# Optimization experiments

Hardware: AMD Instinct MI355X
Metric: run time of the kernel (lower is better)

Reference implementation:

```python
import jax, jax.numpy as jnp
import numpy as np

B, L, D = 4, 2048, 2048
H, KVH = 16, 4
HD = D // H            # 128
G = H // KVH           # GQA group size
K_SEL = L // 4         # top_k_ratio = 0.25 -> 512
MAX_SEQ = 8192
THETA = 10000.0
SCALE = HD ** -0.5
NEG = -1e9


def _rope_tables(dim, max_len, theta):
    inv = 1.0 / theta ** (jnp.arange(0, dim, 2, dtype=jnp.float32) / dim)  # (dim/2,)
    ang = jnp.arange(max_len, dtype=jnp.float32)[:, None] * inv[None, :]   # (max_len, dim/2)
    return jnp.cos(ang), jnp.sin(ang)


def _apply_rope_pos(x, cos, sin, pos):
    # x: (B, h, K, HD), pos: (B, K) int positions
    c = cos[pos][:, None]  # (B,1,K,HD/2)
    s = sin[pos][:, None]
    x1, x2 = jnp.split(x, 2, axis=-1)
    return jnp.concatenate([x1 * c - x2 * s, x1 * s + x2 * c], axis=-1)


def setup_inputs() -> dict:
    key = jax.random.key(0)
    ks = jax.random.split(key, 8)
    std = 0.02
    x   = jax.random.normal(ks[0], (B, L, D), dtype=jnp.float32)
    Wq  = jax.random.normal(ks[1], (D, D), dtype=jnp.float32) * std
    Wkv = jax.random.normal(ks[2], (D, 2 * KVH * HD), dtype=jnp.float32) * std
    Wo  = jax.random.normal(ks[3], (D, D), dtype=jnp.float32) * std
    W1  = jax.random.normal(ks[4], (D, D // 4), dtype=jnp.float32) * std
    b1  = jnp.zeros((D // 4,), dtype=jnp.float32)
    W2  = jax.random.normal(ks[5], (D // 4, 1), dtype=jnp.float32) * std
    b2  = jnp.zeros((1,), dtype=jnp.float32)
    return {"x": x, "Wq": Wq, "Wkv": Wkv, "Wo": Wo,
            "W1": W1, "b1": b1, "W2": W2, "b2": b2}


def reference(x, Wq, Wkv, Wo, W1, b1, W2, b2):
    Bx, Lx, Dx = x.shape
    # 1. learned per-token importance scores
    imp = (jax.nn.gelu(x @ W1 + b1, approximate=False) @ W2 + b2)[..., 0]  # (B,L)
    # 2. top-k token selection, sorted to keep original order
    _, idx = jax.lax.top_k(imp, K_SEL)
    idx = jnp.sort(idx, axis=-1)                                           # (B,K)
    x_sel = jnp.take_along_axis(x, idx[..., None], axis=1)                 # (B,K,D)
    # 3. fused KV projection on the selected subset (GQA)
    kv = x_sel @ Wkv
    k, v = jnp.split(kv, 2, axis=-1)
    k = k.reshape(Bx, K_SEL, KVH, HD).transpose(0, 2, 1, 3)                # (B,KVH,K,HD)
    v = v.reshape(Bx, K_SEL, KVH, HD).transpose(0, 2, 1, 3)
    # 4. RoPE with original positions for K, contiguous positions for Q
    cos, sin = _rope_tables(HD, MAX_SEQ, THETA)
    k = _apply_rope_pos(k, cos, sin, idx)
    q = (x @ Wq).reshape(Bx, Lx, H, HD).transpose(0, 2, 1, 3)              # (B,H,L,HD)
    qpos = jnp.broadcast_to(jnp.arange(Lx)[None, :], (Bx, Lx))
    q = _apply_rope_pos(q, cos, sin, qpos)
    # 5. GQA head expansion + attention over gathered keys
    k = jnp.repeat(k, G, axis=1)                                           # (B,H,K,HD)
    v = jnp.repeat(v, G, axis=1)
    scores = jnp.einsum('bhld,bhkd->bhlk', q, k) * SCALE                   # (B,H,L,K)
    # causal mask on original key positions
    causal = idx[:, None, None, :] > jnp.arange(Lx)[None, None, :, None]
    scores = jnp.where(causal, NEG, scores)
    attn = jax.nn.softmax(scores, axis=-1)
    # 6. importance soft gating (gradient path into the scorer)
    gate = jax.nn.sigmoid(jnp.take_along_axis(imp, idx, axis=1))           # (B,K)
    attn = attn * gate[:, None, None, :]
    out = jnp.einsum('bhlk,bhkd->bhld', attn, v)                           # (B,H,L,HD)
    out = out.transpose(0, 2, 1, 3).reshape(Bx, Lx, Dx)
    return out @ Wo
```

## Files before the change

kernel.cpp:

```cpp
#include <hip/hip_runtime.h>
#include <math.h>

typedef unsigned short u16;
typedef __attribute__((ext_vector_type(8))) short short8;
typedef __attribute__((ext_vector_type(4))) float f32x4;

__device__ __forceinline__ float bf2f(u16 u) {
  return __uint_as_float(((unsigned)u) << 16);
}
__device__ __forceinline__ u16 f2bf(float f) {
  unsigned u = __float_as_uint(f);
  return (u16)((u + 0x7fffu + ((u >> 16) & 1u)) >> 16);
}

__device__ __forceinline__ void gload_lds16(const u16* g, u16* l) {
  __builtin_amdgcn_global_load_lds((const __attribute__((address_space(1))) unsigned int*)g,
                                   (__attribute__((address_space(3))) unsigned int*)l, 16, 0, 0);
}

__device__ __forceinline__ void stage_tile(const u16* __restrict__ gbase, int ldg,
                                           u16* lds, int w, int lane) {
  #pragma unroll
  for (int i = 0; i < 4; ++i) {
    int c = w * 4 + i;
    const u16* g = gbase + (size_t)(c * 8 + (lane >> 3)) * ldg + (lane & 7) * 8;
    gload_lds16(g, lds + c * 512);
  }
}

__global__ __launch_bounds__(256) void cvt_x_kernel(const float* __restrict__ x,
                                                    u16* __restrict__ xb,
                                                    u16* __restrict__ xlo) {
  size_t base = ((size_t)blockIdx.x * 256 + threadIdx.x) * 8;
  short8 hi, lo;
  #pragma unroll
  for (int i = 0; i < 8; ++i) {
    float v = x[base + i];
    u16 h = f2bf(v);
    hi[i] = (short)h;
    lo[i] = (short)f2bf(v - bf2f(h));
  }
  *(short8*)&xb[base] = hi;
  *(short8*)&xlo[base] = lo;
}

template <bool HILO>
__global__ __launch_bounds__(256) void transpose_cvt(const float* __restrict__ in,
                                                     u16* __restrict__ outH,
                                                     u16* __restrict__ outL,
                                                     int R, int C) {
  __shared__ u16 tH[64][72];
  __shared__ u16 tL[64][72];
  int rb = blockIdx.y * 64, cb = blockIdx.x * 64;
  int t = threadIdx.x;
  #pragma unroll
  for (int i = 0; i < 16; ++i) {
    int r = i * 4 + (t >> 6), c = t & 63;
    float v = in[(size_t)(rb + r) * C + cb + c];
    u16 h = f2bf(v);
    tH[r][c] = h;
    if (HILO) tL[r][c] = f2bf(v - bf2f(h));
  }
  __syncthreads();
  #pragma unroll
  for (int i = 0; i < 16; ++i) {
    int r = i * 4 + (t >> 6), c = t & 63;
    outH[(size_t)(cb + r) * R + rb + c] = tH[c][r];
    if (HILO) outL[(size_t)(cb + r) * R + rb + c] = tL[c][r];
  }
}

__global__ void ropetab_kernel(float* __restrict__ cosT, float* __restrict__ sinT) {
  int pos = blockIdx.x, i = threadIdx.x;
  float e = (float)(2 * i) * (1.0f / 128.0f);
  float inv = powf(10000.0f, -e);
  float ang = (float)pos * inv;
  cosT[pos * 64 + i] = cosf(ang);
  sinT[pos * 64 + i] = sinf(ang);
}

template <bool BF16OUT>
__global__ __launch_bounds__(512, 2) void gemm256(const u16* __restrict__ A,
                                                  const u16* __restrict__ BT,
                                                  float* __restrict__ Cf,
                                                  u16* __restrict__ Cb,
                                                  int M, int N, int K) {
  __shared__ __align__(1024) u16 smem[65536];
  const int bm = blockIdx.x * 256, bn = blockIdx.y * 256;
  const int t = threadIdx.x, lane = t & 63, w = t >> 6;
  const int ll = lane & 15, lh = lane >> 4;
  const int wr = w >> 2, wc = w & 3;
  const int NT = K >> 6;

  const int tt0 = t, tt1 = t + 512;
  const int r0 = tt0 >> 2, r1 = tt1 >> 2;
  const int c0 = (((tt0 & 3) ^ ((tt0 >> 3) & 3)) << 3);
  const int c1 = (((tt1 & 3) ^ ((tt1 >> 3) & 3)) << 3);
  const size_t aoff0 = (size_t)(bm + r0) * K + c0;
  const size_t aoff1 = (size_t)(bm + r1) * K + c1;
  const size_t boff0 = (size_t)(bn + r0) * K + c0;
  const size_t boff1 = (size_t)(bn + r1) * K + c1;

  const int swz = ((lh ^ ((ll >> 1) & 3)) << 3);
  const int arow = (wr * 128 + ll) * 32 + swz;
  const int brow = (wc * 64 + ll) * 32 + swz;

  f32x4 acc[8][4];
  #pragma unroll
  for (int mi = 0; mi < 8; ++mi)
    #pragma unroll
    for (int ni = 0; ni < 4; ++ni) acc[mi][ni] = f32x4{0.f, 0.f, 0.f, 0.f};

  short8 aq[8], bq[2];

#define G_STAGE(base, o0, o1, lds) \
  gload_lds16((base) + (o0), (lds) + w * 512); \
  gload_lds16((base) + (o1), (lds) + 4096 + w * 512)
#define RD_A(Sa, ks) \
  _Pragma("unroll") for (int mi = 0; mi < 8; ++mi) aq[mi] = *(const short8*)&(Sa)[(ks)*8192 + arow + mi * 512]
#define RD_B(Sb, ks, nh) \
  _Pragma("unroll") for (int n2 = 0; n2 < 2; ++n2) bq[n2] = *(const short8*)&(Sb)[(ks)*8192 + brow + ((nh)*2 + n2) * 512]
#define DO_MFMA(nh) \
  __builtin_amdgcn_s_setprio(1); \
  _Pragma("unroll") for (int mi = 0; mi < 8; ++mi) \
    _Pragma("unroll") for (int n2 = 0; n2 < 2; ++n2) \
      acc[mi][(nh)*2 + n2] = __builtin_amdgcn_mfma_f32_16x16x32_bf16(aq[mi], bq[n2], acc[mi][(nh)*2 + n2], 0, 0, 0); \
  __builtin_amdgcn_s_setprio(0)
#define VMW(n) asm volatile("s_waitcnt vmcnt(" #n ")" ::: "memory")

  G_STAGE(A, aoff0, aoff1, smem);
  G_STAGE(BT, boff0, boff1, smem + 16384);
  G_STAGE(A, aoff0 + 32, aoff1 + 32, smem + 8192);
  G_STAGE(BT, boff0 + 32, boff1 + 32, smem + 16384 + 8192);

  for (int kt = 0; kt < NT - 1; ++kt) {
    const int cur = kt & 1;
    u16* Sa = smem + cur * 32768;
    u16* Sb = Sa + 16384;
    u16* Pa = smem + (cur ^ 1) * 32768;
    u16* Pb = Pa + 16384;
    const size_t kg = (size_t)(kt + 1) * 64;
    VMW(4);
    __builtin_amdgcn_s_barrier();
    G_STAGE(A, aoff0 + kg, aoff1 + kg, Pa);
    RD_A(Sa, 0);
    RD_B(Sb, 0, 0);
    DO_MFMA(0);
    __builtin_amdgcn_s_barrier();
    G_STAGE(BT, boff0 + kg, boff1 + kg, Pb);
    RD_B(Sb, 0, 1);
    DO_MFMA(1);
    VMW(4);
    __builtin_amdgcn_s_barrier();
    G_STAGE(A, aoff0 + kg + 32, aoff1 + kg + 32, Pa + 8192);
    RD_A(Sa, 1);
    RD_B(Sb, 1, 0);
    DO_MFMA(0);
    __builtin_amdgcn_s_barrier();
    G_STAGE(BT, boff0 + kg + 32, boff1 + kg + 32, Pb + 8192);
    RD_B(Sb, 1, 1);
    DO_MFMA(1);
  }
  {
    const int cur = (NT - 1) & 1;
    u16* Sa = smem + cur * 32768;
    u16* Sb = Sa + 16384;
    VMW(4);
    __builtin_amdgcn_s_barrier();
    RD_A(Sa, 0); RD_B(Sb, 0, 0); DO_MFMA(0);
    __builtin_amdgcn_s_barrier();
    RD_B(Sb, 0, 1); DO_MFMA(1);
    VMW(0);
    __builtin_amdgcn_s_barrier();
    RD_A(Sa, 1); RD_B(Sb, 1, 0); DO_MFMA(0);
    __builtin_amdgcn_s_barrier();
    RD_B(Sb, 1, 1); DO_MFMA(1);
  }

  #pragma unroll
  for (int mi = 0; mi < 8; ++mi)
    #pragma unroll
    for (int ni = 0; ni < 4; ++ni)
      #pragma unroll
      for (int r = 0; r < 4; ++r) {
        int row = bm + wr * 128 + mi * 16 + lh * 4 + r;
        int col = bn + wc * 64 + ni * 16 + ll;
        float v = acc[mi][ni][r];
        if (BF16OUT) Cb[(size_t)row * N + col] = f2bf(v);
        else Cf[(size_t)row * N + col] = v;
      }
#undef G_STAGE
#undef RD_A
#undef RD_B
#undef DO_MFMA
#undef VMW
}

__global__ __launch_bounds__(256) void gemm_bt_gather(const u16* __restrict__ A,
                                                      const u16* __restrict__ BT,
                                                      const int* __restrict__ rowidx,
                                                      float* __restrict__ Cpart,
                                                      int M, int N, int K) {
  constexpr int BK = 64;
  __shared__ u16 As[128][BK + 8];
  __shared__ u16 Bs[128][BK + 8];
  const int bm = blockIdx.x * 128, bn = blockIdx.y * 128;
  const int kz = blockIdx.z;
  const int t = threadIdx.x, lane = t & 63, w = t >> 6;
  const int lh = lane >> 4, ll = lane & 15;
  const int wm = (w >> 1) * 64, wn = (w & 1) * 64;
  f32x4 acc[4][4];
  #pragma unroll
  for (int mt = 0; mt < 4; ++mt)
    #pragma unroll
    for (int nt = 0; nt < 4; ++nt) acc[mt][nt] = f32x4{0.f, 0.f, 0.f, 0.f};

  const int k0 = kz * (K / 2), k1 = k0 + K / 2;
  for (int kb = k0; kb < k1; kb += BK) {
    __syncthreads();
    #pragma unroll
    for (int i = 0; i < 4; ++i) {
      int e = t + i * 256;
      int row = e >> 3, c8 = e & 7;
      int arow = rowidx[bm + row];
      *(short8*)&As[row][c8 * 8] = *(const short8*)&A[(size_t)arow * K + kb + c8 * 8];
      *(short8*)&Bs[row][c8 * 8] = *(const short8*)&BT[(size_t)(bn + row) * K + kb + c8 * 8];
    }
    __syncthreads();
    #pragma unroll
    for (int ks = 0; ks < 2; ++ks) {
      short8 a[4], b[4];
      #pragma unroll
      for (int mt = 0; mt < 4; ++mt) a[mt] = *(const short8*)&As[wm + mt * 16 + ll][ks * 32 + lh * 8];
      #pragma unroll
      for (int nt = 0; nt < 4; ++nt) b[nt] = *(const short8*)&Bs[wn + nt * 16 + ll][ks * 32 + lh * 8];
      #pragma unroll
      for (int mt = 0; mt < 4; ++mt)
        #pragma unroll
        for (int nt = 0; nt < 4; ++nt)
          acc[mt][nt] = __builtin_amdgcn_mfma_f32_16x16x32_bf16(a[mt], b[nt], acc[mt][nt], 0, 0, 0);
    }
  }
  float* C = Cpart + (size_t)kz * M * N;
  #pragma unroll
  for (int mt = 0; mt < 4; ++mt)
    #pragma unroll
    for (int nt = 0; nt < 4; ++nt)
      #pragma unroll
      for (int r = 0; r < 4; ++r) {
        int row = bm + wm + mt * 16 + lh * 4 + r;
        int col = bn + wn + nt * 16 + ll;
        C[(size_t)row * N + col] = acc[mt][nt][r];
      }
}

__global__ __launch_bounds__(256) void gemm_scorer(const u16* __restrict__ Ahi,
                                                   const u16* __restrict__ Alo,
                                                   const u16* __restrict__ Bhi,
                                                   const u16* __restrict__ Blo,
                                                   float* __restrict__ Cpart,
                                                   int M, int N, int K) {
  __shared__ __align__(1024) u16 smem[4 * 128 * 64];
  u16* AsH = smem;
  u16* AsL = smem + 128 * 64;
  u16* BsH = smem + 2 * 128 * 64;
  u16* BsL = smem + 3 * 128 * 64;
  const int bm = blockIdx.x * 128, bn = blockIdx.y * 128;
  const int kz = blockIdx.z;
  const int t = threadIdx.x, lane = t & 63, w = t >> 6;
  const int lh = lane >> 4, ll = lane & 15;
  const int wm = (w >> 1) * 64, wn = (w & 1) * 64;
  f32x4 acc[4][4];
  #pragma unroll
  for (int mt = 0; mt < 4; ++mt)
    #pragma unroll
    for (int nt = 0; nt < 4; ++nt) acc[mt][nt] = f32x4{0.f, 0.f, 0.f, 0.f};

  const int k0 = kz * (K / 2), k1 = k0 + K / 2;
  for (int kb = k0; kb < k1; kb += 64) {
    __syncthreads();
    stage_tile(Ahi + (size_t)bm * K + kb, K, AsH, w, lane);
    stage_tile(Alo + (size_t)bm * K + kb, K, AsL, w, lane);
    stage_tile(Bhi + (size_t)bn * K + kb, K, BsH, w, lane);
    stage_tile(Blo + (size_t)bn * K + kb, K, BsL, w, lane);
    __syncthreads();
    #pragma unroll
    for (int ks = 0; ks < 2; ++ks) {
      short8 ah[4], al[4], bh[4], bl[4];
      #pragma unroll
      for (int mt = 0; mt < 4; ++mt) {
        int o = (wm + mt * 16 + ll) * 64 + ks * 32 + lh * 8;
        ah[mt] = *(const short8*)&AsH[o];
        al[mt] = *(const short8*)&AsL[o];
      }
      #pragma unroll
      for (int nt = 0; nt < 4; ++nt) {
        int o = (wn + nt * 16 + ll) * 64 + ks * 32 + lh * 8;
        bh[nt] = *(const short8*)&BsH[o];
        bl[nt] = *(const short8*)&BsL[o];
      }
      #pragma unroll
      for (int mt = 0; mt < 4; ++mt)
        #pragma unroll
        for (int nt = 0; nt < 4; ++nt) {
          acc[mt][nt] = __builtin_amdgcn_mfma_f32_16x16x32_bf16(ah[mt], bh[nt], acc[mt][nt], 0, 0, 0);
          acc[mt][nt] = __builtin_amdgcn_mfma_f32_16x16x32_bf16(ah[mt], bl[nt], acc[mt][nt], 0, 0, 0);
          acc[mt][nt] = __builtin_amdgcn_mfma_f32_16x16x32_bf16(al[mt], bh[nt], acc[mt][nt], 0, 0, 0);
        }
    }
  }
  float* C = Cpart + (size_t)kz * M * N;
  #pragma unroll
  for (int mt = 0; mt < 4; ++mt)
    #pragma unroll
    for (int nt = 0; nt < 4; ++nt)
      #pragma unroll
      for (int r = 0; r < 4; ++r) {
        int row = bm + wm + mt * 16 + lh * 4 + r;
        int col = bn + wn + nt * 16 + ll;
        C[(size_t)row * N + col] = acc[mt][nt][r];
      }
}

__global__ __launch_bounds__(256) void scorer_finish(const float* __restrict__ hg,
                                                     const float* __restrict__ b1,
                                                     const float* __restrict__ W2,
                                                     const float* __restrict__ b2,
                                                     float* __restrict__ imp) {
  int tok = blockIdx.x * 4 + (threadIdx.x >> 6);
  int lane = threadIdx.x & 63;
  const float* h0 = hg + (size_t)tok * 512;
  const float* h1 = hg + (size_t)8192 * 512 + (size_t)tok * 512;
  float s = 0.f;
  #pragma unroll
  for (int i = 0; i < 8; ++i) {
    int c = lane + i * 64;
    float v = h0[c] + h1[c] + b1[c];
    v = 0.5f * v * (1.0f + erff(v * 0.70710678118654752f));
    s += v * W2[c];
  }
  #pragma unroll
  for (int off = 32; off; off >>= 1) s += __shfl_xor(s, off, 64);
  if (lane == 0) imp[tok] = s + b2[0];
}

__global__ __launch_bounds__(1024) void topk_kernel(const float* __restrict__ imp,
                                                    int* __restrict__ idx_sel,
                                                    int* __restrict__ sel_rows,
                                                    float* __restrict__ gatev) {
  __shared__ float v[2048];
  __shared__ int ix[2048];
  __shared__ int ids[512];
  int b = blockIdx.x, t = threadIdx.x;
  for (int i = t; i < 2048; i += 1024) { v[i] = imp[b * 2048 + i]; ix[i] = i; }
  __syncthreads();
  for (int k = 2; k <= 2048; k <<= 1)
    for (int j = k >> 1; j > 0; j >>= 1) {
      int i = ((t & ~(j - 1)) << 1) | (t & (j - 1));
      int l2 = i | j;
      bool dir = ((i & k) == 0);
      float vi = v[i], vl = v[l2];
      int xi = ix[i], xl = ix[l2];
      bool g = (vi < vl) || (vi == vl && xi > xl);
      if (g == dir) { v[i] = vl; v[l2] = vi; ix[i] = xl; ix[l2] = xi; }
      __syncthreads();
    }
  if (t < 512) ids[t] = ix[t];
  __syncthreads();
  for (int k = 2; k <= 512; k <<= 1)
    for (int j = k >> 1; j > 0; j >>= 1) {
      if (t < 256) {
        int i = ((t & ~(j - 1)) << 1) | (t & (j - 1));
        int l2 = i | j;
        bool dir = ((i & k) == 0);
        int ai = ids[i], al = ids[l2];
        if ((ai > al) == dir) { ids[i] = al; ids[l2] = ai; }
      }
      __syncthreads();
    }
  if (t < 512) {
    int id = ids[t];
    idx_sel[b * 512 + t] = id;
    sel_rows[b * 512 + t] = b * 2048 + id;
    float g = imp[b * 2048 + id];
    gatev[b * 512 + t] = 1.0f / (1.0f + __expf(-g));
  }
}

__global__ __launch_bounds__(256) void rope_k2(const float* __restrict__ part,
                                               const int* __restrict__ idx_sel,
                                               const float* __restrict__ cosT,
                                               const float* __restrict__ sinT,
                                               u16* __restrict__ Kb) {
  int gid = blockIdx.x * 256 + threadIdx.x;
  int i = gid & 63;
  int s = (gid >> 6) & 511;
  int kvh = (gid >> 15) & 3;
  int b = gid >> 17;
  size_t src = (size_t)(b * 512 + s) * 1024 + kvh * 128 + i;
  float k1 = part[src] + part[src + 2097152];
  float k2 = part[src + 64] + part[src + 64 + 2097152];
  int pos = idx_sel[b * 512 + s];
  float c = cosT[pos * 64 + i], sn = sinT[pos * 64 + i];
  size_t dst = (size_t)((b * 4 + kvh) * 512 + s) * 128 + i;
  Kb[dst] = f2bf(k1 * c - k2 * sn);
  Kb[dst + 64] = f2bf(k1 * sn + k2 * c);
}

__global__ __launch_bounds__(256) void vtrans2(const float* __restrict__ part,
                                               const float* __restrict__ gatev,
                                               u16* __restrict__ VT) {
  int gid = blockIdx.x * 256 + threadIdx.x;
  int s = gid & 511;
  int d = (gid >> 9) & 127;
  int kvh = (gid >> 16) & 3;
  int b = gid >> 18;
  size_t src = (size_t)(b * 512 + s) * 1024 + 512 + kvh * 128 + d;
  float v = part[src] + part[src + 2097152];
  VT[(size_t)((b * 4 + kvh) * 128 + d) * 512 + s] = f2bf(v * gatev[b * 512 + s]);
}

__global__ __launch_bounds__(512) void attn_kernel(const u16* __restrict__ Qb,
                                                   const u16* __restrict__ Kb,
                                                   const u16* __restrict__ VTb,
                                                   const int* __restrict__ idxp,
                                                   const float* __restrict__ cosT,
                                                   const float* __restrict__ sinT,
                                                   u16* __restrict__ Ob) {
  __shared__ u16 Ks[64][132];
  __shared__ u16 Vs[128][76];
  __shared__ u16 Ps[8][16][68];
  __shared__ int idx_s[64];

  const int qt = (blockIdx.x + 4 * blockIdx.z) & 15;
  const int h = blockIdx.y, b = blockIdx.z;
  const int kvh = h >> 2;
  const int t = threadIdx.x, lane = t & 63, w = t >> 6;
  const int lh = lane >> 4, ll = lane & 15;
  const int q0 = qt * 128;
  const float SCALE_LOG2E = 0.12753102331f;

  int NT = 8;
  if (idxp[b * 512] <= q0) {
    NT = 1;
    while (NT < 8 && idxp[b * 512 + NT * 64] <= q0 + 127) ++NT;
  }

  const int lrow = q0 + w * 16 + ll;
  short8 aq[4];
  #pragma unroll
  for (int ks = 0; ks < 4; ++ks)
    aq[ks] = *(const short8*)&Qb[(size_t)(b * 2048 + lrow) * 2048 + h * 128 + ks * 32 + lh * 8];
  {
    const float* cp = cosT + (size_t)lrow * 64 + lh * 8;
    const float* sp = sinT + (size_t)lrow * 64 + lh * 8;
    short8 n0, n1, n2, n3;
    #pragma unroll
    for (int j = 0; j < 8; ++j) {
      float cA = cp[j], sA = sp[j], cB = cp[32 + j], sB = sp[32 + j];
      float x0 = bf2f((u16)aq[0][j]), x2 = bf2f((u16)aq[2][j]);
      float x1 = bf2f((u16)aq[1][j]), x3 = bf2f((u16)aq[3][j]);
      n0[j] = (short)f2bf(x0 * cA - x2 * sA);
      n2[j] = (short)f2bf(x0 * sA + x2 * cA);
      n1[j] = (short)f2bf(x1 * cB - x3 * sB);
      n3[j] = (short)f2bf(x1 * sB + x3 * cB);
    }
    aq[0] = n0; aq[1] = n1; aq[2] = n2; aq[3] = n3;
  }

  float m[4], lden[4];
  f32x4 O[8];
  #pragma unroll
  for (int r = 0; r < 4; ++r) { m[r] = -INFINITY; lden[r] = 0.f; }
  #pragma unroll
  for (int dt = 0; dt < 8; ++dt) O[dt] = f32x4{0.f, 0.f, 0.f, 0.f};

  for (int kt = 0; kt < NT; ++kt) {
    const int tmax = idxp[b * 512 + kt * 64 + 63];
    const bool nomask = (tmax <= q0 + w * 16);

    __syncthreads();
    #pragma unroll
    for (int i = 0; i < 2; ++i) {
      int e = t + i * 512;
      int krow = e >> 4, kc8 = e & 15;
      *(short8*)&Ks[krow][kc8 * 8] =
          *(const short8*)&Kb[(size_t)((b * 4 + kvh) * 512 + kt * 64 + krow) * 128 + kc8 * 8];
      int vrow = e >> 3, vc8 = e & 7;
      *(short8*)&Vs[vrow][vc8 * 8] =
          *(const short8*)&VTb[(size_t)((b * 4 + kvh) * 128 + vrow) * 512 + kt * 64 + vc8 * 8];
    }
    if (t < 64) idx_s[t] = idxp[b * 512 + kt * 64 + t];
    __syncthreads();

    f32x4 S[4];
    #pragma unroll
    for (int nt = 0; nt < 4; ++nt) S[nt] = f32x4{0.f, 0.f, 0.f, 0.f};
    #pragma unroll
    for (int nt = 0; nt < 4; ++nt)
      #pragma unroll
      for (int ks = 0; ks < 4; ++ks) {
        short8 bk = *(const short8*)&Ks[nt * 16 + ll][ks * 32 + lh * 8];
        S[nt] = __builtin_amdgcn_mfma_f32_16x16x32_bf16(aq[ks], bk, S[nt], 0, 0, 0);
      }

    float p[4][4], lmax[4];
    #pragma unroll
    for (int r = 0; r < 4; ++r) lmax[r] = -INFINITY;
    if (nomask) {
      #pragma unroll
      for (int nt = 0; nt < 4; ++nt)
        #pragma unroll
        for (int r = 0; r < 4; ++r) {
          float s = S[nt][r] * SCALE_LOG2E;
          p[nt][r] = s;
          lmax[r] = fmaxf(lmax[r], s);
        }
    } else {
      #pragma unroll
      for (int nt = 0; nt < 4; ++nt) {
        int kpos = idx_s[nt * 16 + ll];
        #pragma unroll
        for (int r = 0; r < 4; ++r) {
          int row = q0 + w * 16 + lh * 4 + r;
          float s = S[nt][r] * SCALE_LOG2E;
          if (kpos > row) s = -1e9f;
          p[nt][r] = s;
          lmax[r] = fmaxf(lmax[r], s);
        }
      }
    }
    #pragma unroll
    for (int off = 8; off; off >>= 1)
      #pragma unroll
      for (int r = 0; r < 4; ++r) lmax[r] = fmaxf(lmax[r], __shfl_xor(lmax[r], off, 64));

    bool need = false;
    #pragma unroll
    for (int r = 0; r < 4; ++r) need = need || (lmax[r] > m[r] + 8.0f);
    if (__any(need)) {
      #pragma unroll
      for (int r = 0; r < 4; ++r) {
        float mnew = fmaxf(m[r], lmax[r]);
        float alpha = exp2f(m[r] - mnew);
        m[r] = mnew;
        lden[r] *= alpha;
        #pragma unroll
        for (int dt = 0; dt < 8; ++dt) O[dt][r] *= alpha;
      }
    }

    float rs[4] = {0.f, 0.f, 0.f, 0.f};
    #pragma unroll
    for (int nt = 0; nt < 4; ++nt)
      #pragma unroll
      for (int r = 0; r < 4; ++r) {
        float e = exp2f(p[nt][r] - m[r]);
        p[nt][r] = e;
        rs[r] += e;
      }
    #pragma unroll
    for (int off = 8; off; off >>= 1)
      #pragma unroll
      for (int r = 0; r < 4; ++r) rs[r] += __shfl_xor(rs[r], off, 64);
    #pragma unroll
    for (int r = 0; r < 4; ++r) lden[r] += rs[r];

    #pragma unroll
    for (int nt = 0; nt < 4; ++nt)
      #pragma unroll
      for (int r = 0; r < 4; r += 2) {
        unsigned pk;
        asm("v_cvt_pk_bf16_f32 %0, %1, %2" : "=v"(pk) : "v"(p[nt][r]), "v"(p[nt][r + 1]));
        Ps[w][lh * 4 + r][nt * 16 + ll] = (u16)pk;
        Ps[w][lh * 4 + r + 1][nt * 16 + ll] = (u16)(pk >> 16);
      }
    #pragma unroll
    for (int ks = 0; ks < 2; ++ks) {
      short8 pa = *(const short8*)&Ps[w][ll][ks * 32 + lh * 8];
      #pragma unroll
      for (int dt = 0; dt < 8; ++dt) {
        short8 vb = *(const short8*)&Vs[dt * 16 + ll][ks * 32 + lh * 8];
        O[dt] = __builtin_amdgcn_mfma_f32_16x16x32_bf16(pa, vb, O[dt], 0, 0, 0);
      }
    }
  }

  #pragma unroll
  for (int dt = 0; dt < 8; ++dt)
    #pragma unroll
    for (int r = 0; r < 4; ++r) {
      int row = q0 + w * 16 + lh * 4 + r;
      int col = h * 128 + dt * 16 + ll;
      Ob[(size_t)(b * 2048 + row) * 2048 + col] = f2bf(O[dt][r] / lden[r]);
    }
}

extern "C" void kernel_launch(void* const* d_in, const int* in_sizes, int n_in,
                              void* d_out, int out_size, void* d_ws, size_t ws_size,
                              hipStream_t stream) {
  const float* x = (const float*)d_in[0];
  const float* Wq = (const float*)d_in[1];
  const float* Wkv = (const float*)d_in[2];
  const float* Wo = (const float*)d_in[3];
  const float* W1 = (const float*)d_in[4];
  const float* b1 = (const float*)d_in[5];
  const float* W2 = (const float*)d_in[6];
  const float* b2 = (const float*)d_in[7];
  float* out = (float*)d_out;

  char* ws = (char*)d_ws;
  size_t off = 0;
  auto alloc = [&](size_t bytes) {
    char* p = ws + off;
    off = (off + bytes + 255) & ~(size_t)255;
    return p;
  };
  u16* xb = (u16*)alloc((size_t)8192 * 2048 * 2);
  u16* xlo = (u16*)alloc((size_t)8192 * 2048 * 2);
  u16* W1Th = (u16*)alloc((size_t)512 * 2048 * 2);
  u16* W1Tl = (u16*)alloc((size_t)512 * 2048 * 2);
  u16* WqT = (u16*)alloc((size_t)2048 * 2048 * 2);
  u16* WkvT = (u16*)alloc((size_t)1024 * 2048 * 2);
  u16* WoT = (u16*)alloc((size_t)2048 * 2048 * 2);
  float* cosT = (float*)alloc((size_t)2048 * 64 * 4);
  float* sinT = (float*)alloc((size_t)2048 * 64 * 4);
  float* hg = (float*)alloc((size_t)2 * 8192 * 512 * 4);
  float* impv = (float*)alloc((size_t)8192 * 4);
  int* idx_sel = (int*)alloc((size_t)2048 * 4);
  int* sel_rows = (int*)alloc((size_t)2048 * 4);
  float* gatev = (float*)alloc((size_t)2048 * 4);
  u16* qbuf = (u16*)alloc((size_t)8192 * 2048 * 2);
  u16* Kbuf = (u16*)alloc((size_t)4 * 4 * 512 * 128 * 2);
  u16* VTbuf = (u16*)alloc((size_t)4 * 4 * 128 * 512 * 2);
  u16* attn_out = xlo;
  float* kvpart = hg;

  cvt_x_kernel<<<8192, 256, 0, stream>>>(x, xb, xlo);
  transpose_cvt<true><<<dim3(512 / 64, 2048 / 64), 256, 0, stream>>>(W1, W1Th, W1Tl, 2048, 512);
  transpose_cvt<false><<<dim3(32, 32), 256, 0, stream>>>(Wq, WqT, nullptr, 2048, 2048);
  transpose_cvt<false><<<dim3(16, 32), 256, 0, stream>>>(Wkv, WkvT, nullptr, 2048, 1024);
  transpose_cvt<false><<<dim3(32, 32), 256, 0, stream>>>(Wo, WoT, nullptr, 2048, 2048);
  ropetab_kernel<<<2048, 64, 0, stream>>>(cosT, sinT);

  gemm_scorer<<<dim3(64, 4, 2), 256, 0, stream>>>(xb, xlo, W1Th, W1Tl, hg, 8192, 512, 2048);
  scorer_finish<<<2048, 256, 0, stream>>>(hg, b1, W2, b2, impv);
  topk_kernel<<<4, 1024, 0, stream>>>(impv, idx_sel, sel_rows, gatev);

  gemm256<true><<<dim3(32, 8), 512, 0, stream>>>(xb, WqT, nullptr, qbuf, 8192, 2048, 2048);

  gemm_bt_gather<<<dim3(16, 8, 2), 256, 0, stream>>>(xb, WkvT, sel_rows, kvpart, 2048, 1024, 2048);
  rope_k2<<<2048, 256, 0, stream>>>(kvpart, idx_sel, cosT, sinT, Kbuf);
  vtrans2<<<4096, 256, 0, stream>>>(kvpart, gatev, VTbuf);

  attn_kernel<<<dim3(16, 16, 4), 512, 0, stream>>>(qbuf, Kbuf, VTbuf, idx_sel, cosT, sinT, attn_out);

  gemm256<false><<<dim3(32, 8), 512, 0, stream>>>(attn_out, WoT, out, nullptr, 8192, 2048, 2048);
}
```

Before: 384.1 us.

## Rewrite scorer GEMM with double-buffered async LDS loads and swizzled 256x128 tiles

```diff
diff --git a/kernel.cpp b/kernel.cpp
--- a/kernel.cpp
+++ b/kernel.cpp
@@ -254,72 +254,108 @@
       }
 }
 
-__global__ __launch_bounds__(256) void gemm_scorer(const u16* __restrict__ Ahi,
+__global__ __launch_bounds__(512) void gemm_scorer(const u16* __restrict__ Ahi,
                                                    const u16* __restrict__ Alo,
                                                    const u16* __restrict__ Bhi,
                                                    const u16* __restrict__ Blo,
                                                    float* __restrict__ Cpart,
                                                    int M, int N, int K) {
-  __shared__ __align__(1024) u16 smem[4 * 128 * 64];
-  u16* AsH = smem;
-  u16* AsL = smem + 128 * 64;
-  u16* BsH = smem + 2 * 128 * 64;
-  u16* BsL = smem + 3 * 128 * 64;
-  const int bm = blockIdx.x * 128, bn = blockIdx.y * 128;
+  __shared__ __align__(1024) u16 smem[49152];
+  const int bm = blockIdx.x * 256, bn = blockIdx.y * 128;
   const int kz = blockIdx.z;
   const int t = threadIdx.x, lane = t & 63, w = t >> 6;
-  const int lh = lane >> 4, ll = lane & 15;
-  const int wm = (w >> 1) * 64, wn = (w & 1) * 64;
-  f32x4 acc[4][4];
-  #pragma unroll
-  for (int mt = 0; mt < 4; ++mt)
-    #pragma unroll
-    for (int nt = 0; nt < 4; ++nt) acc[mt][nt] = f32x4{0.f, 0.f, 0.f, 0.f};
-
-  const int k0 = kz * (K / 2), k1 = k0 + K / 2;
-  for (int kb = k0; kb < k1; kb += 64) {
-    __syncthreads();
-    stage_tile(Ahi + (size_t)bm * K + kb, K, AsH, w, lane);
-    stage_tile(Alo + (size_t)bm * K + kb, K, AsL, w, lane);
-    stage_tile(Bhi + (size_t)bn * K + kb, K, BsH, w, lane);
-    stage_tile(Blo + (size_t)bn * K + kb, K, BsL, w, lane);
-    __syncthreads();
-    #pragma unroll
-    for (int ks = 0; ks < 2; ++ks) {
-      short8 ah[4], al[4], bh[4], bl[4];
-      #pragma unroll
-      for (int mt = 0; mt < 4; ++mt) {
-        int o = (wm + mt * 16 + ll) * 64 + ks * 32 + lh * 8;
-        ah[mt] = *(const short8*)&AsH[o];
-        al[mt] = *(const short8*)&AsL[o];
-      }
-      #pragma unroll
-      for (int nt = 0; nt < 4; ++nt) {
-        int o = (wn + nt * 16 + ll) * 64 + ks * 32 + lh * 8;
-        bh[nt] = *(const short8*)&BsH[o];
-        bl[nt] = *(const short8*)&BsL[o];
-      }
-      #pragma unroll
-      for (int mt = 0; mt < 4; ++mt)
-        #pragma unroll
-        for (int nt = 0; nt < 4; ++nt) {
-          acc[mt][nt] = __builtin_amdgcn_mfma_f32_16x16x32_bf16(ah[mt], bh[nt], acc[mt][nt], 0, 0, 0);
-          acc[mt][nt] = __builtin_amdgcn_mfma_f32_16x16x32_bf16(ah[mt], bl[nt], acc[mt][nt], 0, 0, 0);
-          acc[mt][nt] = __builtin_amdgcn_mfma_f32_16x16x32_bf16(al[mt], bh[nt], acc[mt][nt], 0, 0, 0);
-        }
-    }
-  }
+  const int ll = lane & 15, lh = lane >> 4;
+  const int wr = w >> 2, wc = w & 3;
+
+  const int cA0 = (w * 2) * 64 + lane;
+  const int cA1 = (w * 2 + 1) * 64 + lane;
+  const int cB = w * 64 + lane;
+  const size_t offA0 = (size_t)(bm + (cA0 >> 2)) * K + (((cA0 & 3) ^ ((cA0 >> 3) & 3)) << 3);
+  const size_t offA1 = (size_t)(bm + (cA1 >> 2)) * K + (((cA1 & 3) ^ ((cA1 >> 3) & 3)) << 3);
+  const size_t offB = (size_t)(bn + (cB >> 2)) * K + (((cB & 3) ^ ((cB >> 3) & 3)) << 3);
+
+  const int arow = wr * 128 + ll;
+  const int brow = wc * 32 + ll;
+
+  f32x4 acc[8][2];
+  #pragma unroll
+  for (int mi = 0; mi < 8; ++mi)
+    #pragma unroll
+    for (int ni = 0; ni < 2; ++ni) acc[mi][ni] = f32x4{0.f, 0.f, 0.f, 0.f};
+
+#define S_STAGE(buf, kb) \
+  gload_lds16(Ahi + offA0 + (kb), (buf) + cA0 * 8); \
+  gload_lds16(Ahi + offA1 + (kb), (buf) + cA1 * 8); \
+  gload_lds16(Alo + offA0 + (kb), (buf) + 8192 + cA0 * 8); \
+  gload_lds16(Alo + offA1 + (kb), (buf) + 8192 + cA1 * 8); \
+  gload_lds16(Bhi + offB + (kb), (buf) + 16384 + cB * 8); \
+  gload_lds16(Blo + offB + (kb), (buf) + 20480 + cB * 8)
+#define SVMW(n) asm volatile("s_waitcnt vmcnt(" #n ")" ::: "memory")
+
+  const int k0 = kz * (K / 2);
+  const int NT = (K / 2) / 32;
+
+  S_STAGE(smem, k0);
+
+  for (int kt = 0; kt < NT; ++kt) {
+    const int cur = kt & 1;
+    u16* S = smem + cur * 24576;
+    SVMW(0);
+    __builtin_amdgcn_s_barrier();
+    if (kt + 1 < NT) { S_STAGE(smem + (cur ^ 1) * 24576, k0 + (kt + 1) * 32); }
+
+    short8 aH[8], aL[8], bH[2], bL[2];
+    #pragma unroll
+    for (int mi = 0; mi < 8; ++mi) {
+      int r = arow + mi * 16;
+      int o = r * 32 + ((lh ^ ((r >> 1) & 3)) << 3);
+      aH[mi] = *(const short8*)&S[o];
+      aL[mi] = *(const short8*)&S[8192 + o];
+    }
+    #pragma unroll
+    for (int ni = 0; ni < 2; ++ni) {
+      int r = brow + ni * 16;
+      int o = r * 32 + ((lh ^ ((r >> 1) & 3)) << 3);
+      bH[ni] = *(const short8*)&S[16384 + o];
+      bL[ni] = *(const short8*)&S[20480 + o];
+    }
+    __builtin_amdgcn_s_setprio(1);
+    #pragma unroll
+    for (int mi = 0; mi < 8; ++mi)
+      #pragma unroll
+      for (int ni = 0; ni < 2; ++ni)
+        acc[mi][ni] = __builtin_amdgcn_mfma_f32_16x16x32_bf16(aH[mi], bH[ni], acc[mi][ni], 0, 0, 0);
+    __builtin_amdgcn_s_setprio(0);
+    __builtin_amdgcn_s_setprio(1);
+    #pragma unroll
+    for (int mi = 0; mi < 8; ++mi)
+      #pragma unroll
+      for (int ni = 0; ni < 2; ++ni)
+        acc[mi][ni] = __builtin_amdgcn_mfma_f32_16x16x32_bf16(aH[mi], bL[ni], acc[mi][ni], 0, 0, 0);
+    __builtin_amdgcn_s_setprio(0);
+    __builtin_amdgcn_s_setprio(1);
+    #pragma unroll
+    for (int mi = 0; mi < 8; ++mi)
+      #pragma unroll
+      for (int ni = 0; ni < 2; ++ni)
+        acc[mi][ni] = __builtin_amdgcn_mfma_f32_16x16x32_bf16(aL[mi], bH[ni], acc[mi][ni], 0, 0, 0);
+    __builtin_amdgcn_s_setprio(0);
+    __builtin_amdgcn_s_barrier();
+  }
+
   float* C = Cpart + (size_t)kz * M * N;
   #pragma unroll
-  for (int mt = 0; mt < 4; ++mt)
-    #pragma unroll
-    for (int nt = 0; nt < 4; ++nt)
+  for (int mi = 0; mi < 8; ++mi)
+    #pragma unroll
+    for (int ni = 0; ni < 2; ++ni)
       #pragma unroll
       for (int r = 0; r < 4; ++r) {
-        int row = bm + wm + mt * 16 + lh * 4 + r;
-        int col = bn + wn + nt * 16 + ll;
-        C[(size_t)row * N + col] = acc[mt][nt][r];
-      }
+        int row = bm + wr * 128 + mi * 16 + lh * 4 + r;
+        int col = bn + wc * 32 + ni * 16 + ll;
+        C[(size_t)row * N + col] = acc[mi][ni][r];
+      }
+#undef S_STAGE
+#undef SVMW
 }
 
 __global__ __launch_bounds__(256) void scorer_finish(const float* __restrict__ hg,
@@ -643,7 +679,7 @@
   transpose_cvt<false><<<dim3(32, 32), 256, 0, stream>>>(Wo, WoT, nullptr, 2048, 2048);
   ropetab_kernel<<<2048, 64, 0, stream>>>(cosT, sinT);
 
-  gemm_scorer<<<dim3(64, 4, 2), 256, 0, stream>>>(xb, xlo, W1Th, W1Tl, hg, 8192, 512, 2048);
+  gemm_scorer<<<dim3(32, 4, 2), 512, 0, stream>>>(xb, xlo, W1Th, W1Tl, hg, 8192, 512, 2048);
   scorer_finish<<<2048, 256, 0, stream>>>(hg, b1, W2, b2, impv);
   topk_kernel<<<4, 1024, 0, stream>>>(impv, idx_sel, sel_rows, gatev);
 
```

Measured after the change: 382.3 us. Within noise of the previous version (-0.5%).
